# Kernel tuning notes

Hardware: AMD Instinct MI355X
Metric: run time of the kernel (lower is better)

## Reference

```python
import jax, jax.numpy as jnp
import numpy as np

TAU = 0.5
N, D = 8192, 128


def _l2norm(x):
    return x / jnp.linalg.norm(x, axis=-1, keepdims=True)


def setup_inputs() -> dict:
    key = jax.random.key(0)
    k1, k2 = jax.random.split(key)
    # Projected + L2-normalized node embeddings (output of GRACE._encode)
    z1 = _l2norm(jax.random.normal(k1, (N, D), dtype=jnp.float32))
    z2 = _l2norm(jax.random.normal(k2, (N, D), dtype=jnp.float32))
    return {"z1": z1, "z2": z2}


def reference(z1, z2):
    # refl_sim = exp(z1 z1^T / tau), between_sim = exp(z1 z2^T / tau)
    refl = jnp.exp(jnp.matmul(z1, z1.T) / TAU)        # [N, N]
    between = jnp.exp(jnp.matmul(z1, z2.T) / TAU)     # [N, N]

    def half_loss(a, b):
        # positives = diag(b); negatives = off-diag of a and b per row.
        # denom = (rowsum(a) - diag(a)) + (rowsum(b) - diag(b)) + diag(b)
        pos = jnp.diagonal(b)
        denom = a.sum(axis=1) - jnp.diagonal(a) + b.sum(axis=1)
        return -jnp.log(pos / denom)

    l1 = half_loss(refl, between)      # row view
    l2 = half_loss(refl.T, between.T)  # column view (diag is shared)
    ret = 0.5 * (l1 + l2)
    return ret.mean()
```

## Files before the change

### kernel.cpp

```cpp
#include <hip/hip_runtime.h>

typedef __attribute__((ext_vector_type(8))) short bf16x8;
typedef __attribute__((ext_vector_type(4))) float f32x4;
typedef unsigned short u16;

constexpr int N = 8192;
constexpr int D = 128;
constexpr float CEXP   = 2.8853900817779268f;
constexpr float BSCALE = 1.6986435688113073f;

#if __has_builtin(__builtin_amdgcn_exp2f)
__device__ __forceinline__ float fexp2(float x) { return __builtin_amdgcn_exp2f(x); }
#else
__device__ __forceinline__ float fexp2(float x) { return exp2f(x); }
#endif

__device__ __forceinline__ u16 f2bf(float x) {
  union { float f; unsigned u; } v;
  v.f = x;
  unsigned r = v.u + 0x7fffu + ((v.u >> 16) & 1u);
  return (u16)(r >> 16);
}

__global__ void convert_kernel(const float4* __restrict__ z1, const float4* __restrict__ z2,
                               uint2* __restrict__ o1, uint2* __restrict__ o2) {
  int t = blockIdx.x * 256 + threadIdx.x;
  float4 a = z1[t];
  float4 b = z2[t];
  uint2 pa, pb;
  pa.x = (unsigned)f2bf(a.x * BSCALE) | ((unsigned)f2bf(a.y * BSCALE) << 16);
  pa.y = (unsigned)f2bf(a.z * BSCALE) | ((unsigned)f2bf(a.w * BSCALE) << 16);
  pb.x = (unsigned)f2bf(b.x * BSCALE) | ((unsigned)f2bf(b.y * BSCALE) << 16);
  pb.y = (unsigned)f2bf(b.z * BSCALE) | ((unsigned)f2bf(b.w * BSCALE) << 16);
  o1[t] = pa;
  o2[t] = pb;
}

__global__ void zero_kernel(float* __restrict__ p, float* __restrict__ out) {
  int g = blockIdx.x * 256 + threadIdx.x;
  p[g] = 0.0f;
  if (g == 0) out[0] = 0.0f;
}

__device__ __forceinline__ void stage32k(char* lds, const char* gsrc, int soff, int doff) {
#pragma unroll
  for (int s = 0; s < 8; ++s) {
    __builtin_amdgcn_global_load_lds(
        (const __attribute__((address_space(1))) unsigned*)(gsrc + soff + s * 4096),
        (__attribute__((address_space(3))) unsigned*)(lds + doff + s * 4096), 16, 0, 0);
  }
}

__global__ __launch_bounds__(256, 2) void gemm_kernel(const u16* __restrict__ z1b,
                                                      const u16* __restrict__ z2b,
                                                      float* __restrict__ rowRefl,
                                                      float* __restrict__ rowBet,
                                                      float* __restrict__ colBet) {
  __shared__ __align__(16) char B0[32768];
  __shared__ __align__(16) char B1[32768];
  const int tid = threadIdx.x;
  const int l = tid & 63, w = tid >> 6;
  const int wr = w >> 1, wc = w & 1;
  const int lr = l & 15, lg = l >> 4;
  const int bi = blockIdx.x >> 3, jg = blockIdx.x & 7;
  const bool between = (jg & 4) != 0;
  const u16* bsrc = between ? z2b : z1b;
  const int j0 = (jg & 3) * 16;

  const int soff = (tid >> 4) * 256 + (((tid & 15) ^ (tid >> 4)) << 4);
  const int doff = tid * 16;

  stage32k(B0, (const char*)(z1b + (size_t)bi * 128 * D), soff, doff);
  __syncthreads();
  bf16x8 af[4][4];
#pragma unroll
  for (int m = 0; m < 4; ++m) {
    const int row = wr * 64 + m * 16 + lr;
#pragma unroll
    for (int kk = 0; kk < 4; ++kk)
      af[m][kk] = *(const bf16x8*)(B0 + row * 256 + (((kk * 4 + lg) ^ lr) << 4));
  }
  __syncthreads();

  stage32k(B0, (const char*)(bsrc + (size_t)j0 * 128 * D), soff, doff);

  float rowp[4][4];
#pragma unroll
  for (int m = 0; m < 4; ++m)
#pragma unroll
    for (int r = 0; r < 4; ++r) rowp[m][r] = 0.f;

  for (int t = 0; t < 16; ++t) {
    __syncthreads();
    const char* cur = (t & 1) ? B1 : B0;
    char* nxt = (t & 1) ? B0 : B1;
    if (t + 1 < 16)
      stage32k(nxt, (const char*)(bsrc + (size_t)(j0 + t + 1) * 128 * D), soff, doff);

    f32x4 acc[4][4];
    const f32x4 z4 = {0.f, 0.f, 0.f, 0.f};
    {
      bf16x8 bfr[4];
#pragma unroll
      for (int n = 0; n < 4; ++n) {
        const int row = wc * 64 + n * 16 + lr;
        bfr[n] = *(const bf16x8*)(cur + row * 256 + ((lg ^ lr) << 4));
      }
#pragma unroll
      for (int m = 0; m < 4; ++m)
#pragma unroll
        for (int n = 0; n < 4; ++n)
          acc[m][n] = __builtin_amdgcn_mfma_f32_16x16x32_bf16(af[m][0], bfr[n], z4, 0, 0, 0);
    }
#pragma unroll
    for (int kk = 1; kk < 4; ++kk) {
      bf16x8 bfr[4];
#pragma unroll
      for (int n = 0; n < 4; ++n) {
        const int row = wc * 64 + n * 16 + lr;
        bfr[n] = *(const bf16x8*)(cur + row * 256 + (((kk * 4 + lg) ^ lr) << 4));
      }
#pragma unroll
      for (int m = 0; m < 4; ++m)
#pragma unroll
        for (int n = 0; n < 4; ++n)
          acc[m][n] = __builtin_amdgcn_mfma_f32_16x16x32_bf16(af[m][kk], bfr[n], acc[m][n], 0, 0, 0);
    }

    if (!between) {
#pragma unroll
      for (int m = 0; m < 4; ++m)
#pragma unroll
        for (int n = 0; n < 4; ++n)
#pragma unroll
          for (int r = 0; r < 4; ++r) rowp[m][r] += fexp2(acc[m][n][r]);
    } else {
      float colp[4];
#pragma unroll
      for (int n = 0; n < 4; ++n) colp[n] = 0.f;
#pragma unroll
      for (int m = 0; m < 4; ++m)
#pragma unroll
        for (int n = 0; n < 4; ++n) {
          float v0 = fexp2(acc[m][n][0]), v1 = fexp2(acc[m][n][1]);
          float v2 = fexp2(acc[m][n][2]), v3 = fexp2(acc[m][n][3]);
          rowp[m][0] += v0;
          rowp[m][1] += v1;
          rowp[m][2] += v2;
          rowp[m][3] += v3;
          colp[n] += (v0 + v1) + (v2 + v3);
        }
#pragma unroll
      for (int n = 0; n < 4; ++n) {
        float c = colp[n];
        c += __shfl_xor(c, 16);
        c += __shfl_xor(c, 32);
        if (l < 16) atomicAdd(&colBet[(size_t)(j0 + t) * 128 + wc * 64 + n * 16 + l], c);
      }
    }
  }

  float* rowdst = between ? rowBet : rowRefl;
#pragma unroll
  for (int m = 0; m < 4; ++m)
#pragma unroll
    for (int r = 0; r < 4; ++r) {
      float s = rowp[m][r];
      s += __shfl_xor(s, 1);
      s += __shfl_xor(s, 2);
      s += __shfl_xor(s, 4);
      s += __shfl_xor(s, 8);
      if (lr == 0) atomicAdd(&rowdst[bi * 128 + wr * 64 + m * 16 + lg * 4 + r], s);
    }
}

__global__ void row_loss_kernel(const float* __restrict__ z1, const float* __restrict__ z2,
                                const float* __restrict__ rowRefl, const float* __restrict__ rowBet,
                                const float* __restrict__ colBet, float* __restrict__ rowLoss) {
  int gt = blockIdx.x * blockDim.x + threadIdx.x;
  int w = gt >> 6;
  int l = threadIdx.x & 63;
  if (w >= N) return;
  float a0 = z1[w * D + l], a1 = z1[w * D + 64 + l];
  float b0 = z2[w * D + l], b1 = z2[w * D + 64 + l];
  float d11 = a0 * a0 + a1 * a1;
  float d12 = a0 * b0 + a1 * b1;
#pragma unroll
  for (int mask = 1; mask < 64; mask <<= 1) {
    d11 += __shfl_xor(d11, mask);
    d12 += __shfl_xor(d12, mask);
  }
  if (l == 0) {
    float rdiag = fexp2(d11 * CEXP);
    float denom1 = rowRefl[w] - rdiag + rowBet[w];
    float denom2 = rowRefl[w] - rdiag + colBet[w];
    rowLoss[w] = 0.5f * (logf(denom1) + logf(denom2)) - 2.0f * d12;
  }
}

__global__ void final_reduce_kernel(const float* __restrict__ rowLoss, float* __restrict__ out) {
  int g = blockIdx.x * 256 + threadIdx.x;
  float s = rowLoss[g] * (1.0f / (float)N);
#pragma unroll
  for (int mask = 1; mask < 64; mask <<= 1) s += __shfl_xor(s, mask);
  if ((threadIdx.x & 63) == 0) atomicAdd(out, s);
}

extern "C" void kernel_launch(void* const* d_in, const int* in_sizes, int n_in,
                              void* d_out, int out_size, void* d_ws, size_t ws_size,
                              hipStream_t stream) {
  const float* z1 = (const float*)d_in[0];
  const float* z2 = (const float*)d_in[1];
  float* out = (float*)d_out;
  char* ws = (char*)d_ws;

  u16* z1b = (u16*)ws;
  u16* z2b = (u16*)(ws + (size_t)N * D * 2);
  float* rowRefl = (float*)(ws + (size_t)2 * N * D * 2);
  float* rowBet = rowRefl + N;
  float* colBet = rowBet + N;
  float* rowLoss = colBet + N;

  convert_kernel<<<(N * D / 4) / 256, 256, 0, stream>>>((const float4*)z1, (const float4*)z2,
                                                        (uint2*)z1b, (uint2*)z2b);
  zero_kernel<<<(3 * N) / 256, 256, 0, stream>>>(rowRefl, out);
  gemm_kernel<<<512, 256, 0, stream>>>(z1b, z2b, rowRefl, rowBet, colBet);
  row_loss_kernel<<<(N * 64) / 256, 256, 0, stream>>>(z1, z2, rowRefl, rowBet, colBet, rowLoss);
  final_reduce_kernel<<<32, 256, 0, stream>>>(rowLoss, out);
}
```

Before: 63.57 us.

## Drop LDS staging in GEMM, fuse convert/zero/dot kernels, merge final reduction

The GEMM kernel no longer stages B tiles through LDS with async global-to-LDS copies and double buffering. Each wave now loads its own 16-column B fragments directly from global memory, with 64-row A blocks and 2048 blocks at 4 blocks per CU. Convert, zeroing and the diagonal dot products are fused into one kernel, and the row-loss and final reduction are merged, cutting five launches to three. The GEMM relies on L2/cache for B reuse instead of shared memory, so it risks more global traffic and exposed load latency. It also issues more column atomics.

```diff
diff --git a/kernel.cpp b/kernel.cpp
--- a/kernel.cpp
+++ b/kernel.cpp
@@ -3,6 +3,7 @@
 typedef __attribute__((ext_vector_type(8))) short bf16x8;
 typedef __attribute__((ext_vector_type(4))) float f32x4;
 typedef unsigned short u16;
+typedef unsigned int u32;
 
 constexpr int N = 8192;
 constexpr int D = 128;
@@ -15,74 +16,65 @@
 __device__ __forceinline__ float fexp2(float x) { return exp2f(x); }
 #endif
 
-__device__ __forceinline__ u16 f2bf(float x) {
+__device__ __forceinline__ u32 f2bf(float x) {
   union { float f; unsigned u; } v;
   v.f = x;
   unsigned r = v.u + 0x7fffu + ((v.u >> 16) & 1u);
-  return (u16)(r >> 16);
+  return r >> 16;
 }
 
-__global__ void convert_kernel(const float4* __restrict__ z1, const float4* __restrict__ z2,
-                               uint2* __restrict__ o1, uint2* __restrict__ o2) {
-  int t = blockIdx.x * 256 + threadIdx.x;
-  float4 a = z1[t];
-  float4 b = z2[t];
-  uint2 pa, pb;
-  pa.x = (unsigned)f2bf(a.x * BSCALE) | ((unsigned)f2bf(a.y * BSCALE) << 16);
-  pa.y = (unsigned)f2bf(a.z * BSCALE) | ((unsigned)f2bf(a.w * BSCALE) << 16);
-  pb.x = (unsigned)f2bf(b.x * BSCALE) | ((unsigned)f2bf(b.y * BSCALE) << 16);
-  pb.y = (unsigned)f2bf(b.z * BSCALE) | ((unsigned)f2bf(b.w * BSCALE) << 16);
-  o1[t] = pa;
-  o2[t] = pb;
-}
+__global__ void convert_dots_kernel(const float2* __restrict__ z1, const float2* __restrict__ z2,
+                                    u32* __restrict__ o1, u32* __restrict__ o2,
+                                    float* __restrict__ dotSelf, float* __restrict__ dotCross,
+                                    float* __restrict__ zeroBase, float* __restrict__ out) {
+  const int tid = threadIdx.x;
+  const int row = blockIdx.x * 4 + (tid >> 6);
+  const int l = tid & 63;
+  const int zidx = blockIdx.x * 256 + tid;
+  if (zidx < 3 * N) zeroBase[zidx] = 0.0f;
+  if (zidx == 0) out[0] = 0.0f;
 
-__global__ void zero_kernel(float* __restrict__ p, float* __restrict__ out) {
-  int g = blockIdx.x * 256 + threadIdx.x;
-  p[g] = 0.0f;
-  if (g == 0) out[0] = 0.0f;
-}
+  float2 a = z1[row * 64 + l];
+  float2 b = z2[row * 64 + l];
+  o1[row * 64 + l] = f2bf(a.x * BSCALE) | (f2bf(a.y * BSCALE) << 16);
+  o2[row * 64 + l] = f2bf(b.x * BSCALE) | (f2bf(b.y * BSCALE) << 16);
 
-__device__ __forceinline__ void stage32k(char* lds, const char* gsrc, int soff, int doff) {
+  float d11 = a.x * a.x + a.y * a.y;
+  float d12 = a.x * b.x + a.y * b.y;
 #pragma unroll
-  for (int s = 0; s < 8; ++s) {
-    __builtin_amdgcn_global_load_lds(
-        (const __attribute__((address_space(1))) unsigned*)(gsrc + soff + s * 4096),
-        (__attribute__((address_space(3))) unsigned*)(lds + doff + s * 4096), 16, 0, 0);
+  for (int mask = 1; mask < 64; mask <<= 1) {
+    d11 += __shfl_xor(d11, mask);
+    d12 += __shfl_xor(d12, mask);
+  }
+  if (l == 0) {
+    dotSelf[row] = d11;
+    dotCross[row] = d12;
   }
 }
 
-__global__ __launch_bounds__(256, 2) void gemm_kernel(const u16* __restrict__ z1b,
+__global__ __launch_bounds__(256, 4) void gemm_kernel(const u16* __restrict__ z1b,
                                                       const u16* __restrict__ z2b,
                                                       float* __restrict__ rowRefl,
                                                       float* __restrict__ rowBet,
                                                       float* __restrict__ colBet) {
-  __shared__ __align__(16) char B0[32768];
-  __shared__ __align__(16) char B1[32768];
   const int tid = threadIdx.x;
   const int l = tid & 63, w = tid >> 6;
-  const int wr = w >> 1, wc = w & 1;
   const int lr = l & 15, lg = l >> 4;
-  const int bi = blockIdx.x >> 3, jg = blockIdx.x & 7;
-  const bool between = (jg & 4) != 0;
+  const int bi = blockIdx.x >> 4;
+  const int jg = blockIdx.x & 15;
+  const bool between = jg >= 8;
   const u16* bsrc = between ? z2b : z1b;
-  const int j0 = (jg & 3) * 16;
+  const int col0 = (jg & 7) * 1024 + w * 16;
 
-  const int soff = (tid >> 4) * 256 + (((tid & 15) ^ (tid >> 4)) << 4);
-  const int doff = tid * 16;
-
-  stage32k(B0, (const char*)(z1b + (size_t)bi * 128 * D), soff, doff);
-  __syncthreads();
   bf16x8 af[4][4];
+  {
+    const char* abase = (const char*)(z1b + (size_t)(bi * 64 + lr) * D + lg * 8);
 #pragma unroll
-  for (int m = 0; m < 4; ++m) {
-    const int row = wr * 64 + m * 16 + lr;
+    for (int m = 0; m < 4; ++m)
 #pragma unroll
-    for (int kk = 0; kk < 4; ++kk)
-      af[m][kk] = *(const bf16x8*)(B0 + row * 256 + (((kk * 4 + lg) ^ lr) << 4));
+      for (int kk = 0; kk < 4; ++kk)
+        af[m][kk] = *(const bf16x8*)(abase + m * 16 * 256 + kk * 64);
   }
-  __syncthreads();
-
-  stage32k(B0, (const char*)(bsrc + (size_t)j0 * 128 * D), soff, doff);
 
   float rowp[4][4];
 #pragma unroll
@@ -90,73 +82,45 @@
 #pragma unroll
     for (int r = 0; r < 4; ++r) rowp[m][r] = 0.f;
 
-  for (int t = 0; t < 16; ++t) {
-    __syncthreads();
-    const char* cur = (t & 1) ? B1 : B0;
-    char* nxt = (t & 1) ? B0 : B1;
-    if (t + 1 < 16)
-      stage32k(nxt, (const char*)(bsrc + (size_t)(j0 + t + 1) * 128 * D), soff, doff);
+  const char* bbase = (const char*)bsrc + (size_t)(col0 + lr) * 256 + lg * 16;
 
-    f32x4 acc[4][4];
+  for (int g = 0; g < 16; ++g) {
+    const char* bp = bbase + (size_t)g * 64 * 256;
+    bf16x8 bfr[4];
+#pragma unroll
+    for (int kk = 0; kk < 4; ++kk) bfr[kk] = *(const bf16x8*)(bp + kk * 64);
+
+    f32x4 acc[4];
     const f32x4 z4 = {0.f, 0.f, 0.f, 0.f};
-    {
-      bf16x8 bfr[4];
 #pragma unroll
-      for (int n = 0; n < 4; ++n) {
-        const int row = wc * 64 + n * 16 + lr;
-        bfr[n] = *(const bf16x8*)(cur + row * 256 + ((lg ^ lr) << 4));
-      }
+    for (int m = 0; m < 4; ++m)
+      acc[m] = __builtin_amdgcn_mfma_f32_16x16x32_bf16(af[m][0], bfr[0], z4, 0, 0, 0);
+#pragma unroll
+    for (int kk = 1; kk < 4; ++kk)
 #pragma unroll
       for (int m = 0; m < 4; ++m)
-#pragma unroll
-        for (int n = 0; n < 4; ++n)
-          acc[m][n] = __builtin_amdgcn_mfma_f32_16x16x32_bf16(af[m][0], bfr[n], z4, 0, 0, 0);
-    }
-#pragma unroll
-    for (int kk = 1; kk < 4; ++kk) {
-      bf16x8 bfr[4];
-#pragma unroll
-      for (int n = 0; n < 4; ++n) {
-        const int row = wc * 64 + n * 16 + lr;
-        bfr[n] = *(const bf16x8*)(cur + row * 256 + (((kk * 4 + lg) ^ lr) << 4));
-      }
-#pragma unroll
-      for (int m = 0; m < 4; ++m)
-#pragma unroll
-        for (int n = 0; n < 4; ++n)
-          acc[m][n] = __builtin_amdgcn_mfma_f32_16x16x32_bf16(af[m][kk], bfr[n], acc[m][n], 0, 0, 0);
-    }
+        acc[m] = __builtin_amdgcn_mfma_f32_16x16x32_bf16(af[m][kk], bfr[kk], acc[m], 0, 0, 0);
 
     if (!between) {
 #pragma unroll
       for (int m = 0; m < 4; ++m)
 #pragma unroll
-        for (int n = 0; n < 4; ++n)
+        for (int r = 0; r < 4; ++r) rowp[m][r] += fexp2(acc[m][r]);
+    } else {
+      float colp = 0.f;
 #pragma unroll
-          for (int r = 0; r < 4; ++r) rowp[m][r] += fexp2(acc[m][n][r]);
-    } else {
-      float colp[4];
-#pragma unroll
-      for (int n = 0; n < 4; ++n) colp[n] = 0.f;
-#pragma unroll
-      for (int m = 0; m < 4; ++m)
-#pragma unroll
-        for (int n = 0; n < 4; ++n) {
-          float v0 = fexp2(acc[m][n][0]), v1 = fexp2(acc[m][n][1]);
-          float v2 = fexp2(acc[m][n][2]), v3 = fexp2(acc[m][n][3]);
-          rowp[m][0] += v0;
-          rowp[m][1] += v1;
-          rowp[m][2] += v2;
-          rowp[m][3] += v3;
-          colp[n] += (v0 + v1) + (v2 + v3);
-        }
-#pragma unroll
-      for (int n = 0; n < 4; ++n) {
-        float c = colp[n];
-        c += __shfl_xor(c, 16);
-        c += __shfl_xor(c, 32);
-        if (l < 16) atomicAdd(&colBet[(size_t)(j0 + t) * 128 + wc * 64 + n * 16 + l], c);
+      for (int m = 0; m < 4; ++m) {
+        float v0 = fexp2(acc[m][0]), v1 = fexp2(acc[m][1]);
+        float v2 = fexp2(acc[m][2]), v3 = fexp2(acc[m][3]);
+        rowp[m][0] += v0;
+        rowp[m][1] += v1;
+        rowp[m][2] += v2;
+        rowp[m][3] += v3;
+        colp += (v0 + v1) + (v2 + v3);
       }
+      colp += __shfl_xor(colp, 16);
+      colp += __shfl_xor(colp, 32);
+      if (l < 16) atomicAdd(&colBet[col0 + g * 64 + l], colp);
     }
   }
 
@@ -170,40 +134,21 @@
       s += __shfl_xor(s, 2);
       s += __shfl_xor(s, 4);
       s += __shfl_xor(s, 8);
-      if (lr == 0) atomicAdd(&rowdst[bi * 128 + wr * 64 + m * 16 + lg * 4 + r], s);
+      if (lr == 0) atomicAdd(&rowdst[bi * 64 + m * 16 + lg * 4 + r], s);
     }
 }
 
-__global__ void row_loss_kernel(const float* __restrict__ z1, const float* __restrict__ z2,
-                                const float* __restrict__ rowRefl, const float* __restrict__ rowBet,
-                                const float* __restrict__ colBet, float* __restrict__ rowLoss) {
-  int gt = blockIdx.x * blockDim.x + threadIdx.x;
-  int w = gt >> 6;
-  int l = threadIdx.x & 63;
-  if (w >= N) return;
-  float a0 = z1[w * D + l], a1 = z1[w * D + 64 + l];
-  float b0 = z2[w * D + l], b1 = z2[w * D + 64 + l];
-  float d11 = a0 * a0 + a1 * a1;
-  float d12 = a0 * b0 + a1 * b1;
+__global__ void final_kernel(const float* __restrict__ rowRefl, const float* __restrict__ rowBet,
+                             const float* __restrict__ colBet, const float* __restrict__ dotSelf,
+                             const float* __restrict__ dotCross, float* __restrict__ out) {
+  const int r = blockIdx.x * 256 + threadIdx.x;
+  float rdiag = fexp2(dotSelf[r] * CEXP);
+  float base = rowRefl[r] - rdiag;
+  float loss = 0.5f * (logf(base + rowBet[r]) + logf(base + colBet[r])) - 2.0f * dotCross[r];
+  loss *= (1.0f / (float)N);
 #pragma unroll
-  for (int mask = 1; mask < 64; mask <<= 1) {
-    d11 += __shfl_xor(d11, mask);
-    d12 += __shfl_xor(d12, mask);
-  }
-  if (l == 0) {
-    float rdiag = fexp2(d11 * CEXP);
-    float denom1 = rowRefl[w] - rdiag + rowBet[w];
-    float denom2 = rowRefl[w] - rdiag + colBet[w];
-    rowLoss[w] = 0.5f * (logf(denom1) + logf(denom2)) - 2.0f * d12;
-  }
-}
-
-__global__ void final_reduce_kernel(const float* __restrict__ rowLoss, float* __restrict__ out) {
-  int g = blockIdx.x * 256 + threadIdx.x;
-  float s = rowLoss[g] * (1.0f / (float)N);
-#pragma unroll
-  for (int mask = 1; mask < 64; mask <<= 1) s += __shfl_xor(s, mask);
-  if ((threadIdx.x & 63) == 0) atomicAdd(out, s);
+  for (int mask = 1; mask < 64; mask <<= 1) loss += __shfl_xor(loss, mask);
+  if ((threadIdx.x & 63) == 0) atomicAdd(out, loss);
 }
 
 extern "C" void kernel_launch(void* const* d_in, const int* in_sizes, int n_in,
@@ -219,12 +164,12 @@
   float* rowRefl = (float*)(ws + (size_t)2 * N * D * 2);
   float* rowBet = rowRefl + N;
   float* colBet = rowBet + N;
-  float* rowLoss = colBet + N;
+  float* dotSelf = colBet + N;
+  float* dotCross = dotSelf + N;
 
-  convert_kernel<<<(N * D / 4) / 256, 256, 0, stream>>>((const float4*)z1, (const float4*)z2,
-                                                        (uint2*)z1b, (uint2*)z2b);
-  zero_kernel<<<(3 * N) / 256, 256, 0, stream>>>(rowRefl, out);
-  gemm_kernel<<<512, 256, 0, stream>>>(z1b, z2b, rowRefl, rowBet, colBet);
-  row_loss_kernel<<<(N * 64) / 256, 256, 0, stream>>>(z1, z2, rowRefl, rowBet, colBet, rowLoss);
-  final_reduce_kernel<<<32, 256, 0, stream>>>(rowLoss, out);
+  convert_dots_kernel<<<N / 4, 256, 0, stream>>>((const float2*)z1, (const float2*)z2,
+                                                 (u32*)z1b, (u32*)z2b, dotSelf, dotCross,
+                                                 rowRefl, out);
+  gemm_kernel<<<2048, 256, 0, stream>>>(z1b, z2b, rowRefl, rowBet, colBet);
+  final_kernel<<<N / 256, 256, 0, stream>>>(rowRefl, rowBet, colBet, dotSelf, dotCross, out);
 }
```

Measured after the change: 99.03 us. +55.8%, slower.
